# Performance work log

Hardware: AMD Instinct MI355X
Metric: run time of the kernel (lower is better)

Reference implementation:

```python
import jax, jax.numpy as jnp
import numpy as np

K = 3           # kernel_size
PAD = (K - 1) // 2
GC = 16         # group_channels (hardcoded in module)
EPS = 1e-5      # BatchNorm eps


def _extract_patches(x):
    # x: [B,C,H,W] -> [B,C,K*K,H,W], patch index = kh*K+kw (torch Unfold order)
    B, C, H, W = x.shape
    xp = jnp.pad(x, ((0, 0), (0, 0), (PAD, PAD), (PAD, PAD)))
    slices = [xp[:, :, i:i + H, j:j + W] for i in range(K) for j in range(K)]
    return jnp.stack(slices, axis=2)


def setup_inputs() -> dict:
    key = jax.random.key(0)
    ks = jax.random.split(key, 6)
    B, C, H, W = 4, 256, 128, 128
    Cr = C // 4                 # reduction_ratio = 4
    G = C // GC                 # groups = 16
    x = jax.random.normal(ks[0], (B, C, H, W), dtype=jnp.float32)
    # conv1: 1x1, C -> C/4, bias-free (followed by BN) + ReLU
    w1 = jax.random.normal(ks[1], (Cr, C), dtype=jnp.float32) * (1.0 / np.sqrt(C))
    bn_gamma = jnp.ones((Cr,), jnp.float32)
    bn_beta = jnp.zeros((Cr,), jnp.float32)
    bn_mean = jax.random.normal(ks[2], (Cr,), dtype=jnp.float32) * 0.1
    bn_var = jax.random.uniform(ks[3], (Cr,), dtype=jnp.float32, minval=0.5, maxval=1.5)
    # conv2: 1x1, C/4 -> K*K*groups, with bias, no norm/act
    w2 = jax.random.normal(ks[4], (K * K * G, Cr), dtype=jnp.float32) * (1.0 / np.sqrt(Cr))
    b2 = jax.random.normal(ks[5], (K * K * G,), dtype=jnp.float32) * 0.01
    return {"x": x, "w1": w1, "bn_gamma": bn_gamma, "bn_beta": bn_beta,
            "bn_mean": bn_mean, "bn_var": bn_var, "w2": w2, "b2": b2}


def reference(x, w1, bn_gamma, bn_beta, bn_mean, bn_var, w2, b2):
    B, C, H, W = x.shape
    G = C // GC
    # conv1 (1x1) + BN (inference) + ReLU
    h1 = jnp.einsum('bchw,oc->bohw', x, w1)
    inv_std = jax.lax.rsqrt(bn_var + EPS)
    h1 = (h1 - bn_mean[None, :, None, None]) * (bn_gamma * inv_std)[None, :, None, None] \
         + bn_beta[None, :, None, None]
    h1 = jax.nn.relu(h1)
    # conv2 (1x1) -> per-pixel dynamic kernels [B, G, K*K, H, W]
    wk = jnp.einsum('bchw,oc->bohw', h1, w2) + b2[None, :, None, None]
    wk = wk.reshape(B, G, K * K, H, W)
    # unfold x -> [B, G, GC, K*K, H, W], multiply by kernels and reduce over K*K
    patches = _extract_patches(x).reshape(B, G, GC, K * K, H, W)
    out = jnp.einsum('bgkhw,bgckhw->bgchw', wk, patches)
    return out.reshape(B, C, H, W)
```

## Files before the change

kernel.cpp:

```cpp
#include <hip/hip_runtime.h>

#define B_   4
#define C_   256
#define CR_  64
#define H_   128
#define W_   128
#define HW_  (H_ * W_)
#define G_   16
#define GC_  16
#define KO_  144
#define EPS_ 1e-5f

typedef __bf16 bf16x8 __attribute__((ext_vector_type(8)));
typedef __bf16 bf16x4 __attribute__((ext_vector_type(4)));
typedef float  f32x4  __attribute__((ext_vector_type(4)));

#define SX2 132
#define WKS 132

__global__ void prep_kernel(const float* __restrict__ w1,
                            const float* __restrict__ gamma,
                            const float* __restrict__ beta,
                            const float* __restrict__ mean,
                            const float* __restrict__ var,
                            const float* __restrict__ w2,
                            __bf16* __restrict__ w1frag,
                            __bf16* __restrict__ w2frag,
                            float* __restrict__ bias2) {
    int idx = blockIdx.x * 256 + threadIdx.x;
    if (idx < 16384) {
        int kc = idx >> 11, r = idx & 2047;
        int mt = r >> 9, l = (r >> 3) & 63, j = r & 7;
        int o = mt * 16 + (l & 15);
        int c = kc * 32 + 8 * (l >> 4) + j;
        float alpha = gamma[o] * rsqrtf(var[o] + EPS_);
        w1frag[idx] = (__bf16)(w1[o * C_ + c] * alpha);
        if (idx < CR_) {
            float a2 = gamma[idx] * rsqrtf(var[idx] + EPS_);
            bias2[idx] = beta[idx] - mean[idx] * a2;
        }
    } else if (idx < 16384 + 9216) {
        int i2 = idx - 16384;
        int mt = i2 >> 10, r = i2 & 1023;
        int kc2 = r >> 9, l = (r >> 3) & 63, j = r & 7;
        int o2 = mt * 16 + (l & 15);
        int cc = kc2 * 32 + 8 * (l >> 4) + j;
        w2frag[i2] = (__bf16)(w2[o2 * CR_ + cc]);
    }
}

__global__ __launch_bounds__(512, 4) void fused_kernel(
        const float* __restrict__ x,
        const __bf16* __restrict__ w1frag,
        const float* __restrict__ bias2,
        const __bf16* __restrict__ w2frag,
        const float* __restrict__ b2,
        float* __restrict__ out) {
    __shared__ __align__(16) char smem[54912];
    __bf16* wkbuf = (__bf16*)smem;
    __bf16* xs    = (__bf16*)smem;
    __bf16* hbuf  = (__bf16*)(smem + 38016);

    const int tid  = threadIdx.x;
    const int lane = tid & 63;
    const int wave = tid >> 6;
    const int wm = wave >> 2, wn = wave & 3;
    const int g = lane >> 4, n = lane & 15;

    const int bid = (blockIdx.x & 7) * 64 + (blockIdx.x >> 3);
    const int b   = bid >> 7;
    const int h   = bid & 127;

    const float* xrow = x + (size_t)b * C_ * HW_ + h * W_;

#pragma unroll
    for (int i = 0; i < 2; ++i) {
        int s = tid + 512 * i;
        int cl = s >> 5, f4i = s & 31;
        float4 v = *(const float4*)&xrow[(size_t)cl * HW_ + f4i * 4];
        *(bf16x4*)&xs[cl * SX2 + f4i * 4] =
            bf16x4{(__bf16)v.x, (__bf16)v.y, (__bf16)v.z, (__bf16)v.w};
    }
    __syncthreads();

    f32x4 acc1[2][2];
#pragma unroll
    for (int m = 0; m < 2; ++m)
#pragma unroll
        for (int t = 0; t < 2; ++t) acc1[m][t] = f32x4{0.f, 0.f, 0.f, 0.f};

    for (int kc = 0; kc < 8; ++kc) {
        const int buf = kc & 1;
        float4 nf[2];
        if (kc < 7) {
#pragma unroll
            for (int i = 0; i < 2; ++i) {
                int s = tid + 512 * i;
                int cl = s >> 5, f4i = s & 31;
                nf[i] = *(const float4*)&xrow[(size_t)(32 * (kc + 1) + cl) * HW_ + f4i * 4];
            }
        }
        bf16x8 a0 = *(const bf16x8*)&w1frag[((kc * 4 + 2 * wm + 0) * 64 + lane) * 8];
        bf16x8 a1 = *(const bf16x8*)&w1frag[((kc * 4 + 2 * wm + 1) * 64 + lane) * 8];
        const int base = buf * (32 * SX2);
        bf16x8 bt[2];
#pragma unroll
        for (int t = 0; t < 2; ++t)
#pragma unroll
            for (int j = 0; j < 8; ++j)
                bt[t][j] = xs[base + (8 * g + j) * SX2 + (2 * wn + t) * 16 + n];
#pragma unroll
        for (int t = 0; t < 2; ++t) {
            acc1[0][t] = __builtin_amdgcn_mfma_f32_16x16x32_bf16(a0, bt[t], acc1[0][t], 0, 0, 0);
            acc1[1][t] = __builtin_amdgcn_mfma_f32_16x16x32_bf16(a1, bt[t], acc1[1][t], 0, 0, 0);
        }
        if (kc < 7) {
            const int nb = (buf ^ 1) * (32 * SX2);
#pragma unroll
            for (int i = 0; i < 2; ++i) {
                int s = tid + 512 * i;
                int cl = s >> 5, f4i = s & 31;
                *(bf16x4*)&xs[nb + cl * SX2 + f4i * 4] =
                    bf16x4{(__bf16)nf[i].x, (__bf16)nf[i].y, (__bf16)nf[i].z, (__bf16)nf[i].w};
            }
        }
        __syncthreads();
    }

#pragma unroll
    for (int m = 0; m < 2; ++m) {
        const int Mo = (2 * wm + m) * 16 + 4 * g;
        float4 bv = *(const float4*)&bias2[Mo];
        float bj[4] = {bv.x, bv.y, bv.z, bv.w};
#pragma unroll
        for (int t = 0; t < 2; ++t) {
            const int px = (2 * wn + t) * 16 + n;
#pragma unroll
            for (int j = 0; j < 4; ++j)
                hbuf[(Mo + j) * SX2 + px] = (__bf16)fmaxf(acc1[m][t][j] + bj[j], 0.f);
        }
    }
    __syncthreads();

    f32x4 acc2[9];
#pragma unroll
    for (int m = 0; m < 9; ++m) acc2[m] = f32x4{0.f, 0.f, 0.f, 0.f};

#pragma unroll
    for (int kc2 = 0; kc2 < 2; ++kc2) {
        bf16x8 hb;
#pragma unroll
        for (int j = 0; j < 8; ++j)
            hb[j] = hbuf[(kc2 * 32 + 8 * g + j) * SX2 + wave * 16 + n];
#pragma unroll
        for (int mt = 0; mt < 9; ++mt) {
            bf16x8 a = *(const bf16x8*)&w2frag[((mt * 2 + kc2) * 64 + lane) * 8];
            acc2[mt] = __builtin_amdgcn_mfma_f32_16x16x32_bf16(a, hb, acc2[mt], 0, 0, 0);
        }
    }

#pragma unroll
    for (int mt = 0; mt < 9; ++mt) {
        const int o0 = mt * 16 + 4 * g;
        float4 bv = *(const float4*)&b2[o0];
        float bj[4] = {bv.x, bv.y, bv.z, bv.w};
#pragma unroll
        for (int j = 0; j < 4; ++j)
            wkbuf[(o0 + j) * WKS + wave * 16 + n] = (__bf16)(acc2[mt][j] + bj[j]);
    }
    __syncthreads();

    const int q   = lane & 31;
    const int sub = lane >> 5;
    const int w0  = q * 4;
    const bool ql = (q == 0), qr = (q == 31);
    const bool h0ok = (h > 0), h2ok = (h < H_ - 1);

    for (int half = 0; half < 2; ++half) {
        const int gq = 2 * wave + half;
        float4 wk4[9];
#pragma unroll
        for (int k = 0; k < 9; ++k) {
            bf16x4 v = *(const bf16x4*)&wkbuf[(gq * 9 + k) * WKS + w0];
            wk4[k] = float4{(float)v[0], (float)v[1], (float)v[2], (float)v[3]};
        }
        const int cbase = gq * GC_ + sub;

        float4 bufA[3], bufB[3];
        {
            const float* xc = x + ((size_t)(b * C_ + cbase)) * HW_ + (h - 1) * W_ + w0;
            bufA[0] = h0ok ? *(const float4*)xc : float4{0.f, 0.f, 0.f, 0.f};
            bufA[1] = *(const float4*)(xc + W_);
            bufA[2] = h2ok ? *(const float4*)(xc + 2 * W_) : float4{0.f, 0.f, 0.f, 0.f};
        }
#pragma unroll
        for (int p = 0; p < 8; ++p) {
            float4* cur = (p & 1) ? bufB : bufA;
            float4* nxt = (p & 1) ? bufA : bufB;
            if (p < 7) {
                const float* xc = x + ((size_t)(b * C_ + cbase + 2 * (p + 1))) * HW_ + (h - 1) * W_ + w0;
                nxt[0] = h0ok ? *(const float4*)xc : float4{0.f, 0.f, 0.f, 0.f};
                nxt[1] = *(const float4*)(xc + W_);
                nxt[2] = h2ok ? *(const float4*)(xc + 2 * W_) : float4{0.f, 0.f, 0.f, 0.f};
            }
            float4 acc = {0.f, 0.f, 0.f, 0.f};
#pragma unroll
            for (int dr = 0; dr < 3; ++dr) {
                float4 c = cur[dr];
                float lms = __shfl(c.w, lane - 1);
                float rms = __shfl(c.x, lane + 1);
                float lm = ql ? 0.f : lms;
                float rm = qr ? 0.f : rms;
                float4 t0 = wk4[3 * dr + 0];
                float4 t1 = wk4[3 * dr + 1];
                float4 t2 = wk4[3 * dr + 2];
                acc.x = fmaf(t0.x, lm,  acc.x);
                acc.y = fmaf(t0.y, c.x, acc.y);
                acc.z = fmaf(t0.z, c.y, acc.z);
                acc.w = fmaf(t0.w, c.z, acc.w);
                acc.x = fmaf(t1.x, c.x, acc.x);
                acc.y = fmaf(t1.y, c.y, acc.y);
                acc.z = fmaf(t1.z, c.z, acc.z);
                acc.w = fmaf(t1.w, c.w, acc.w);
                acc.x = fmaf(t2.x, c.y, acc.x);
                acc.y = fmaf(t2.y, c.z, acc.y);
                acc.z = fmaf(t2.z, c.w, acc.z);
                acc.w = fmaf(t2.w, rm,  acc.w);
            }
            f32x4 av = {acc.x, acc.y, acc.z, acc.w};
            __builtin_nontemporal_store(av,
                (f32x4*)&out[((size_t)(b * C_ + cbase + 2 * p)) * HW_ + h * W_ + w0]);
        }
    }
}

extern "C" void kernel_launch(void* const* d_in, const int* in_sizes, int n_in,
                              void* d_out, int out_size, void* d_ws, size_t ws_size,
                              hipStream_t stream) {
    const float* x     = (const float*)d_in[0];
    const float* w1    = (const float*)d_in[1];
    const float* gamma = (const float*)d_in[2];
    const float* beta  = (const float*)d_in[3];
    const float* mean  = (const float*)d_in[4];
    const float* var   = (const float*)d_in[5];
    const float* w2    = (const float*)d_in[6];
    const float* b2    = (const float*)d_in[7];
    float* out = (float*)d_out;

    char* ws = (char*)d_ws;
    __bf16* w1frag = (__bf16*)(ws);
    __bf16* w2frag = (__bf16*)(ws + (32 << 10));
    float*  bias2  = (float*)(ws + (56 << 10));

    hipLaunchKernelGGL(prep_kernel, dim3(100), dim3(256), 0, stream,
                       w1, gamma, beta, mean, var, w2, w1frag, w2frag, bias2);
    hipLaunchKernelGGL(fused_kernel, dim3(512), dim3(512), 0, stream,
                       x, w1frag, bias2, w2frag, b2, out);
}
```

Measured before the change: 43.24 us.

## Split each row into quarter-width tiles with smaller blocks and LDS footprint

Each block now handles a 32-pixel quarter of an image row with 256 threads instead of a full 128-pixel row with 512 threads. The grid grows from 512 to 2048 blocks and shared memory shrinks from about 54KB to about 10KB, which is meant to raise occupancy and spread the memory-bound work better across CUs. The conv2 MFMA tiles are split 5/4 across wave pairs, and the depthwise stage fetches halo pixels at tile edges with scalar loads. The cost is redundant halo reads, uneven wave work in conv2, and an extra barrier.

```diff
diff --git a/kernel.cpp b/kernel.cpp
--- a/kernel.cpp
+++ b/kernel.cpp
@@ -15,8 +15,7 @@
 typedef __bf16 bf16x4 __attribute__((ext_vector_type(4)));
 typedef float  f32x4  __attribute__((ext_vector_type(4)));
 
-#define SX2 132
-#define WKS 132
+#define ST 36
 
 __global__ void prep_kernel(const float* __restrict__ w1,
                             const float* __restrict__ gamma,
@@ -49,188 +48,180 @@
     }
 }
 
-__global__ __launch_bounds__(512, 4) void fused_kernel(
+__global__ __launch_bounds__(256, 6) void fused_kernel(
         const float* __restrict__ x,
         const __bf16* __restrict__ w1frag,
         const float* __restrict__ bias2,
         const __bf16* __restrict__ w2frag,
         const float* __restrict__ b2,
         float* __restrict__ out) {
-    __shared__ __align__(16) char smem[54912];
+    __shared__ __align__(16) char smem[10368];
+    __bf16* xs    = (__bf16*)smem;
+    __bf16* hbuf  = (__bf16*)(smem + 4608);
     __bf16* wkbuf = (__bf16*)smem;
-    __bf16* xs    = (__bf16*)smem;
-    __bf16* hbuf  = (__bf16*)(smem + 38016);
 
     const int tid  = threadIdx.x;
     const int lane = tid & 63;
     const int wave = tid >> 6;
-    const int wm = wave >> 2, wn = wave & 3;
     const int g = lane >> 4, n = lane & 15;
 
-    const int bid = (blockIdx.x & 7) * 64 + (blockIdx.x >> 3);
-    const int b   = bid >> 7;
-    const int h   = bid & 127;
-
-    const float* xrow = x + (size_t)b * C_ * HW_ + h * W_;
-
-#pragma unroll
-    for (int i = 0; i < 2; ++i) {
-        int s = tid + 512 * i;
-        int cl = s >> 5, f4i = s & 31;
+    const int bid = (blockIdx.x & 7) * 256 + (blockIdx.x >> 3);
+    const int b   = bid >> 9;
+    const int rem = bid & 511;
+    const int h   = rem >> 2;
+    const int qt  = rem & 3;
+    const int w0g = qt * 32;
+
+    const float* xrow = x + (size_t)b * C_ * HW_ + h * W_ + w0g;
+    const int cl  = tid >> 3;
+    const int f4i = tid & 7;
+
+    {
         float4 v = *(const float4*)&xrow[(size_t)cl * HW_ + f4i * 4];
-        *(bf16x4*)&xs[cl * SX2 + f4i * 4] =
+        *(bf16x4*)&xs[cl * ST + f4i * 4] =
             bf16x4{(__bf16)v.x, (__bf16)v.y, (__bf16)v.z, (__bf16)v.w};
     }
     __syncthreads();
 
-    f32x4 acc1[2][2];
-#pragma unroll
-    for (int m = 0; m < 2; ++m)
-#pragma unroll
-        for (int t = 0; t < 2; ++t) acc1[m][t] = f32x4{0.f, 0.f, 0.f, 0.f};
+    f32x4 acc1[2];
+    acc1[0] = f32x4{0.f, 0.f, 0.f, 0.f};
+    acc1[1] = f32x4{0.f, 0.f, 0.f, 0.f};
 
     for (int kc = 0; kc < 8; ++kc) {
         const int buf = kc & 1;
-        float4 nf[2];
+        float4 nf;
+        if (kc < 7)
+            nf = *(const float4*)&xrow[(size_t)(32 * (kc + 1) + cl) * HW_ + f4i * 4];
+        bf16x8 a = *(const bf16x8*)&w1frag[((kc * 4 + wave) * 64 + lane) * 8];
+        const int base = buf * (32 * ST);
+        bf16x8 bt[2];
+#pragma unroll
+        for (int t = 0; t < 2; ++t)
+#pragma unroll
+            for (int j = 0; j < 8; ++j)
+                bt[t][j] = xs[base + (8 * g + j) * ST + t * 16 + n];
+        acc1[0] = __builtin_amdgcn_mfma_f32_16x16x32_bf16(a, bt[0], acc1[0], 0, 0, 0);
+        acc1[1] = __builtin_amdgcn_mfma_f32_16x16x32_bf16(a, bt[1], acc1[1], 0, 0, 0);
         if (kc < 7) {
-#pragma unroll
-            for (int i = 0; i < 2; ++i) {
-                int s = tid + 512 * i;
-                int cl = s >> 5, f4i = s & 31;
-                nf[i] = *(const float4*)&xrow[(size_t)(32 * (kc + 1) + cl) * HW_ + f4i * 4];
-            }
-        }
-        bf16x8 a0 = *(const bf16x8*)&w1frag[((kc * 4 + 2 * wm + 0) * 64 + lane) * 8];
-        bf16x8 a1 = *(const bf16x8*)&w1frag[((kc * 4 + 2 * wm + 1) * 64 + lane) * 8];
-        const int base = buf * (32 * SX2);
-        bf16x8 bt[2];
-#pragma unroll
-        for (int t = 0; t < 2; ++t)
-#pragma unroll
-            for (int j = 0; j < 8; ++j)
-                bt[t][j] = xs[base + (8 * g + j) * SX2 + (2 * wn + t) * 16 + n];
-#pragma unroll
-        for (int t = 0; t < 2; ++t) {
-            acc1[0][t] = __builtin_amdgcn_mfma_f32_16x16x32_bf16(a0, bt[t], acc1[0][t], 0, 0, 0);
-            acc1[1][t] = __builtin_amdgcn_mfma_f32_16x16x32_bf16(a1, bt[t], acc1[1][t], 0, 0, 0);
-        }
-        if (kc < 7) {
-            const int nb = (buf ^ 1) * (32 * SX2);
-#pragma unroll
-            for (int i = 0; i < 2; ++i) {
-                int s = tid + 512 * i;
-                int cl = s >> 5, f4i = s & 31;
-                *(bf16x4*)&xs[nb + cl * SX2 + f4i * 4] =
-                    bf16x4{(__bf16)nf[i].x, (__bf16)nf[i].y, (__bf16)nf[i].z, (__bf16)nf[i].w};
-            }
+            const int nb = (buf ^ 1) * (32 * ST);
+            *(bf16x4*)&xs[nb + cl * ST + f4i * 4] =
+                bf16x4{(__bf16)nf.x, (__bf16)nf.y, (__bf16)nf.z, (__bf16)nf.w};
         }
         __syncthreads();
     }
 
-#pragma unroll
-    for (int m = 0; m < 2; ++m) {
-        const int Mo = (2 * wm + m) * 16 + 4 * g;
+    {
+        const int Mo = wave * 16 + 4 * g;
         float4 bv = *(const float4*)&bias2[Mo];
         float bj[4] = {bv.x, bv.y, bv.z, bv.w};
 #pragma unroll
-        for (int t = 0; t < 2; ++t) {
-            const int px = (2 * wn + t) * 16 + n;
+        for (int t = 0; t < 2; ++t)
 #pragma unroll
             for (int j = 0; j < 4; ++j)
-                hbuf[(Mo + j) * SX2 + px] = (__bf16)fmaxf(acc1[m][t][j] + bj[j], 0.f);
-        }
-    }
-    __syncthreads();
-
-    f32x4 acc2[9];
-#pragma unroll
-    for (int m = 0; m < 9; ++m) acc2[m] = f32x4{0.f, 0.f, 0.f, 0.f};
+                hbuf[(Mo + j) * ST + t * 16 + n] = (__bf16)fmaxf(acc1[t][j] + bj[j], 0.f);
+    }
+    __syncthreads();
+
+    const int nt = wave & 1;
+    const int mh = wave >> 1;
+    const int nmt = mh ? 4 : 5;
+    const int mt0 = mh ? 5 : 0;
+
+    f32x4 acc2[5];
+#pragma unroll
+    for (int m = 0; m < 5; ++m) acc2[m] = f32x4{0.f, 0.f, 0.f, 0.f};
 
 #pragma unroll
     for (int kc2 = 0; kc2 < 2; ++kc2) {
         bf16x8 hb;
 #pragma unroll
         for (int j = 0; j < 8; ++j)
-            hb[j] = hbuf[(kc2 * 32 + 8 * g + j) * SX2 + wave * 16 + n];
-#pragma unroll
-        for (int mt = 0; mt < 9; ++mt) {
-            bf16x8 a = *(const bf16x8*)&w2frag[((mt * 2 + kc2) * 64 + lane) * 8];
-            acc2[mt] = __builtin_amdgcn_mfma_f32_16x16x32_bf16(a, hb, acc2[mt], 0, 0, 0);
-        }
-    }
-
-#pragma unroll
-    for (int mt = 0; mt < 9; ++mt) {
-        const int o0 = mt * 16 + 4 * g;
+            hb[j] = hbuf[(kc2 * 32 + 8 * g + j) * ST + nt * 16 + n];
+        for (int im = 0; im < nmt; ++im) {
+            bf16x8 a = *(const bf16x8*)&w2frag[(((mt0 + im) * 2 + kc2) * 64 + lane) * 8];
+            acc2[im] = __builtin_amdgcn_mfma_f32_16x16x32_bf16(a, hb, acc2[im], 0, 0, 0);
+        }
+    }
+    __syncthreads();
+
+    for (int im = 0; im < nmt; ++im) {
+        const int o0 = (mt0 + im) * 16 + 4 * g;
         float4 bv = *(const float4*)&b2[o0];
         float bj[4] = {bv.x, bv.y, bv.z, bv.w};
 #pragma unroll
         for (int j = 0; j < 4; ++j)
-            wkbuf[(o0 + j) * WKS + wave * 16 + n] = (__bf16)(acc2[mt][j] + bj[j]);
-    }
-    __syncthreads();
-
-    const int q   = lane & 31;
-    const int sub = lane >> 5;
-    const int w0  = q * 4;
-    const bool ql = (q == 0), qr = (q == 31);
+            wkbuf[(o0 + j) * ST + nt * 16 + n] = (__bf16)(acc2[im][j] + bj[j]);
+    }
+    __syncthreads();
+
+    const int q8 = tid & 7;
+    const int cp = tid >> 3;
+    const int gq = cp >> 1;
+    const int w0 = q8 * 4;
+    const bool lb = (q8 == 0), rb = (q8 == 7);
+    const bool il = (qt == 0), ir = (qt == 3);
     const bool h0ok = (h > 0), h2ok = (h < H_ - 1);
 
-    for (int half = 0; half < 2; ++half) {
-        const int gq = 2 * wave + half;
-        float4 wk4[9];
-#pragma unroll
-        for (int k = 0; k < 9; ++k) {
-            bf16x4 v = *(const bf16x4*)&wkbuf[(gq * 9 + k) * WKS + w0];
-            wk4[k] = float4{(float)v[0], (float)v[1], (float)v[2], (float)v[3]};
-        }
-        const int cbase = gq * GC_ + sub;
-
-        float4 bufA[3], bufB[3];
-        {
-            const float* xc = x + ((size_t)(b * C_ + cbase)) * HW_ + (h - 1) * W_ + w0;
-            bufA[0] = h0ok ? *(const float4*)xc : float4{0.f, 0.f, 0.f, 0.f};
-            bufA[1] = *(const float4*)(xc + W_);
-            bufA[2] = h2ok ? *(const float4*)(xc + 2 * W_) : float4{0.f, 0.f, 0.f, 0.f};
-        }
-#pragma unroll
-        for (int p = 0; p < 8; ++p) {
-            float4* cur = (p & 1) ? bufB : bufA;
-            float4* nxt = (p & 1) ? bufA : bufB;
-            if (p < 7) {
-                const float* xc = x + ((size_t)(b * C_ + cbase + 2 * (p + 1))) * HW_ + (h - 1) * W_ + w0;
-                nxt[0] = h0ok ? *(const float4*)xc : float4{0.f, 0.f, 0.f, 0.f};
-                nxt[1] = *(const float4*)(xc + W_);
-                nxt[2] = h2ok ? *(const float4*)(xc + 2 * W_) : float4{0.f, 0.f, 0.f, 0.f};
-            }
-            float4 acc = {0.f, 0.f, 0.f, 0.f};
-#pragma unroll
-            for (int dr = 0; dr < 3; ++dr) {
-                float4 c = cur[dr];
-                float lms = __shfl(c.w, lane - 1);
-                float rms = __shfl(c.x, lane + 1);
-                float lm = ql ? 0.f : lms;
-                float rm = qr ? 0.f : rms;
-                float4 t0 = wk4[3 * dr + 0];
-                float4 t1 = wk4[3 * dr + 1];
-                float4 t2 = wk4[3 * dr + 2];
-                acc.x = fmaf(t0.x, lm,  acc.x);
-                acc.y = fmaf(t0.y, c.x, acc.y);
-                acc.z = fmaf(t0.z, c.y, acc.z);
-                acc.w = fmaf(t0.w, c.z, acc.w);
-                acc.x = fmaf(t1.x, c.x, acc.x);
-                acc.y = fmaf(t1.y, c.y, acc.y);
-                acc.z = fmaf(t1.z, c.z, acc.z);
-                acc.w = fmaf(t1.w, c.w, acc.w);
-                acc.x = fmaf(t2.x, c.y, acc.x);
-                acc.y = fmaf(t2.y, c.z, acc.y);
-                acc.z = fmaf(t2.z, c.w, acc.z);
-                acc.w = fmaf(t2.w, rm,  acc.w);
-            }
-            f32x4 av = {acc.x, acc.y, acc.z, acc.w};
-            __builtin_nontemporal_store(av,
-                (f32x4*)&out[((size_t)(b * C_ + cbase + 2 * p)) * HW_ + h * W_ + w0]);
-        }
+    float4 wk4[9];
+#pragma unroll
+    for (int k = 0; k < 9; ++k) {
+        bf16x4 v = *(const bf16x4*)&wkbuf[(gq * 9 + k) * ST + w0];
+        wk4[k] = float4{(float)v[0], (float)v[1], (float)v[2], (float)v[3]};
+    }
+
+    const int ch0 = cp * 8;
+    float4 bufA[3], bufB[3];
+    float  eA[3], eB[3];
+
+    auto LOADCH = [&](int ci, float4* bf, float* e) {
+        const float* xc = x + ((size_t)(b * C_ + ch0 + ci)) * HW_ + (h - 1) * W_ + w0g + w0;
+#pragma unroll
+        for (int dr = 0; dr < 3; ++dr) {
+            const bool ok = (dr == 0) ? h0ok : (dr == 2) ? h2ok : true;
+            const float* rp = xc + dr * W_;
+            bf[dr] = ok ? *(const float4*)rp : float4{0.f, 0.f, 0.f, 0.f};
+            e[dr] = 0.f;
+            if (lb && ok && !il) e[dr] = rp[-1];
+            if (rb && ok && !ir) e[dr] = rp[4];
+        }
+    };
+
+    LOADCH(0, bufA, eA);
+#pragma unroll
+    for (int p = 0; p < 8; ++p) {
+        float4* cur = (p & 1) ? bufB : bufA;
+        float*  ecur = (p & 1) ? eB : eA;
+        if (p < 7) {
+            if (p & 1) LOADCH(p + 1, bufA, eA);
+            else       LOADCH(p + 1, bufB, eB);
+        }
+        float4 acc = {0.f, 0.f, 0.f, 0.f};
+#pragma unroll
+        for (int dr = 0; dr < 3; ++dr) {
+            float4 c = cur[dr];
+            float lms = __shfl(c.w, lane - 1);
+            float rms = __shfl(c.x, lane + 1);
+            float lm = lb ? ecur[dr] : lms;
+            float rm = rb ? ecur[dr] : rms;
+            float4 t0 = wk4[3 * dr + 0];
+            float4 t1 = wk4[3 * dr + 1];
+            float4 t2 = wk4[3 * dr + 2];
+            acc.x = fmaf(t0.x, lm,  acc.x);
+            acc.y = fmaf(t0.y, c.x, acc.y);
+            acc.z = fmaf(t0.z, c.y, acc.z);
+            acc.w = fmaf(t0.w, c.z, acc.w);
+            acc.x = fmaf(t1.x, c.x, acc.x);
+            acc.y = fmaf(t1.y, c.y, acc.y);
+            acc.z = fmaf(t1.z, c.z, acc.z);
+            acc.w = fmaf(t1.w, c.w, acc.w);
+            acc.x = fmaf(t2.x, c.y, acc.x);
+            acc.y = fmaf(t2.y, c.z, acc.y);
+            acc.z = fmaf(t2.z, c.w, acc.z);
+            acc.w = fmaf(t2.w, rm,  acc.w);
+        }
+        f32x4 av = {acc.x, acc.y, acc.z, acc.w};
+        __builtin_nontemporal_store(av,
+            (f32x4*)&out[((size_t)(b * C_ + ch0 + p)) * HW_ + h * W_ + w0g + w0]);
     }
 }
 
@@ -254,6 +245,6 @@
 
     hipLaunchKernelGGL(prep_kernel, dim3(100), dim3(256), 0, stream,
                        w1, gamma, beta, mean, var, w2, w1frag, w2frag, bias2);
-    hipLaunchKernelGGL(fused_kernel, dim3(512), dim3(512), 0, stream,
+    hipLaunchKernelGGL(fused_kernel, dim3(2048), dim3(256), 0, stream,
                        x, w1frag, bias2, w2frag, b2, out);
 }
```

Measured after the change: 101.2 us. 2.34x slower.

## Double block size to 1024 threads and redistribute work across 16 waves

Applied to the files above, without the earlier changes.

Launches the fused kernel with 1024 threads per block instead of 512 and splits every phase across 16 waves. Each wave now does half of the conv1 tile, about half of the conv2 M-tiles (5 or 4), and one group of the dynamic-kernel application instead of two. The goal is more parallelism and latency hiding per row block, with fewer registers per thread. The risks are that launch_bounds(1024,8) may be unachievable given the 54.9KB of LDS per block, which can force register spills, and that residency may drop to fewer blocks per CU.

```diff
diff --git a/kernel.cpp b/kernel.cpp
--- a/kernel.cpp
+++ b/kernel.cpp
@@ -49,7 +49,7 @@
     }
 }
 
-__global__ __launch_bounds__(512, 4) void fused_kernel(
+__global__ __launch_bounds__(1024, 8) void fused_kernel(
         const float* __restrict__ x,
         const __bf16* __restrict__ w1frag,
         const float* __restrict__ bias2,
@@ -64,7 +64,6 @@
     const int tid  = threadIdx.x;
     const int lane = tid & 63;
     const int wave = tid >> 6;
-    const int wm = wave >> 2, wn = wave & 3;
     const int g = lane >> 4, n = lane & 15;
 
     const int bid = (blockIdx.x & 7) * 64 + (blockIdx.x >> 3);
@@ -73,100 +72,89 @@
 
     const float* xrow = x + (size_t)b * C_ * HW_ + h * W_;
 
-#pragma unroll
-    for (int i = 0; i < 2; ++i) {
-        int s = tid + 512 * i;
-        int cl = s >> 5, f4i = s & 31;
+    {
+        int cl = tid >> 5, f4i = tid & 31;
         float4 v = *(const float4*)&xrow[(size_t)cl * HW_ + f4i * 4];
         *(bf16x4*)&xs[cl * SX2 + f4i * 4] =
             bf16x4{(__bf16)v.x, (__bf16)v.y, (__bf16)v.z, (__bf16)v.w};
     }
     __syncthreads();
 
-    f32x4 acc1[2][2];
-#pragma unroll
-    for (int m = 0; m < 2; ++m)
-#pragma unroll
-        for (int t = 0; t < 2; ++t) acc1[m][t] = f32x4{0.f, 0.f, 0.f, 0.f};
+    const int wm  = wave >> 2;
+    const int wn2 = wave & 3;
+
+    f32x4 acc1[2];
+    acc1[0] = f32x4{0.f, 0.f, 0.f, 0.f};
+    acc1[1] = f32x4{0.f, 0.f, 0.f, 0.f};
 
     for (int kc = 0; kc < 8; ++kc) {
         const int buf = kc & 1;
-        float4 nf[2];
+        float4 nf;
         if (kc < 7) {
-#pragma unroll
-            for (int i = 0; i < 2; ++i) {
-                int s = tid + 512 * i;
-                int cl = s >> 5, f4i = s & 31;
-                nf[i] = *(const float4*)&xrow[(size_t)(32 * (kc + 1) + cl) * HW_ + f4i * 4];
-            }
-        }
-        bf16x8 a0 = *(const bf16x8*)&w1frag[((kc * 4 + 2 * wm + 0) * 64 + lane) * 8];
-        bf16x8 a1 = *(const bf16x8*)&w1frag[((kc * 4 + 2 * wm + 1) * 64 + lane) * 8];
+            int cl = tid >> 5, f4i = tid & 31;
+            nf = *(const float4*)&xrow[(size_t)(32 * (kc + 1) + cl) * HW_ + f4i * 4];
+        }
+        bf16x8 a = *(const bf16x8*)&w1frag[((kc * 4 + wm) * 64 + lane) * 8];
         const int base = buf * (32 * SX2);
         bf16x8 bt[2];
 #pragma unroll
         for (int t = 0; t < 2; ++t)
 #pragma unroll
             for (int j = 0; j < 8; ++j)
-                bt[t][j] = xs[base + (8 * g + j) * SX2 + (2 * wn + t) * 16 + n];
-#pragma unroll
-        for (int t = 0; t < 2; ++t) {
-            acc1[0][t] = __builtin_amdgcn_mfma_f32_16x16x32_bf16(a0, bt[t], acc1[0][t], 0, 0, 0);
-            acc1[1][t] = __builtin_amdgcn_mfma_f32_16x16x32_bf16(a1, bt[t], acc1[1][t], 0, 0, 0);
-        }
+                bt[t][j] = xs[base + (8 * g + j) * SX2 + (2 * wn2 + t) * 16 + n];
+        acc1[0] = __builtin_amdgcn_mfma_f32_16x16x32_bf16(a, bt[0], acc1[0], 0, 0, 0);
+        acc1[1] = __builtin_amdgcn_mfma_f32_16x16x32_bf16(a, bt[1], acc1[1], 0, 0, 0);
         if (kc < 7) {
             const int nb = (buf ^ 1) * (32 * SX2);
-#pragma unroll
-            for (int i = 0; i < 2; ++i) {
-                int s = tid + 512 * i;
-                int cl = s >> 5, f4i = s & 31;
-                *(bf16x4*)&xs[nb + cl * SX2 + f4i * 4] =
-                    bf16x4{(__bf16)nf[i].x, (__bf16)nf[i].y, (__bf16)nf[i].z, (__bf16)nf[i].w};
-            }
+            int cl = tid >> 5, f4i = tid & 31;
+            *(bf16x4*)&xs[nb + cl * SX2 + f4i * 4] =
+                bf16x4{(__bf16)nf.x, (__bf16)nf.y, (__bf16)nf.z, (__bf16)nf.w};
         }
         __syncthreads();
     }
 
-#pragma unroll
-    for (int m = 0; m < 2; ++m) {
-        const int Mo = (2 * wm + m) * 16 + 4 * g;
+    {
+        const int Mo = wm * 16 + 4 * g;
         float4 bv = *(const float4*)&bias2[Mo];
         float bj[4] = {bv.x, bv.y, bv.z, bv.w};
 #pragma unroll
         for (int t = 0; t < 2; ++t) {
-            const int px = (2 * wn + t) * 16 + n;
+            const int px = (2 * wn2 + t) * 16 + n;
 #pragma unroll
             for (int j = 0; j < 4; ++j)
-                hbuf[(Mo + j) * SX2 + px] = (__bf16)fmaxf(acc1[m][t][j] + bj[j], 0.f);
+                hbuf[(Mo + j) * SX2 + px] = (__bf16)fmaxf(acc1[t][j] + bj[j], 0.f);
         }
     }
     __syncthreads();
 
-    f32x4 acc2[9];
-#pragma unroll
-    for (int m = 0; m < 9; ++m) acc2[m] = f32x4{0.f, 0.f, 0.f, 0.f};
+    const int nt  = wave & 7;
+    const int mh  = wave >> 3;
+    const int nmt = mh ? 4 : 5;
+    const int mt0 = mh ? 5 : 0;
+
+    f32x4 acc2[5];
+#pragma unroll
+    for (int m = 0; m < 5; ++m) acc2[m] = f32x4{0.f, 0.f, 0.f, 0.f};
 
 #pragma unroll
     for (int kc2 = 0; kc2 < 2; ++kc2) {
         bf16x8 hb;
 #pragma unroll
         for (int j = 0; j < 8; ++j)
-            hb[j] = hbuf[(kc2 * 32 + 8 * g + j) * SX2 + wave * 16 + n];
-#pragma unroll
-        for (int mt = 0; mt < 9; ++mt) {
-            bf16x8 a = *(const bf16x8*)&w2frag[((mt * 2 + kc2) * 64 + lane) * 8];
-            acc2[mt] = __builtin_amdgcn_mfma_f32_16x16x32_bf16(a, hb, acc2[mt], 0, 0, 0);
-        }
-    }
-
-#pragma unroll
-    for (int mt = 0; mt < 9; ++mt) {
-        const int o0 = mt * 16 + 4 * g;
+            hb[j] = hbuf[(kc2 * 32 + 8 * g + j) * SX2 + nt * 16 + n];
+        for (int im = 0; im < nmt; ++im) {
+            bf16x8 a = *(const bf16x8*)&w2frag[(((mt0 + im) * 2 + kc2) * 64 + lane) * 8];
+            acc2[im] = __builtin_amdgcn_mfma_f32_16x16x32_bf16(a, hb, acc2[im], 0, 0, 0);
+        }
+    }
+
+    for (int im = 0; im < nmt; ++im) {
+        const int o0 = (mt0 + im) * 16 + 4 * g;
         float4 bv = *(const float4*)&b2[o0];
         float bj[4] = {bv.x, bv.y, bv.z, bv.w};
 #pragma unroll
         for (int j = 0; j < 4; ++j)
-            wkbuf[(o0 + j) * WKS + wave * 16 + n] = (__bf16)(acc2[mt][j] + bj[j]);
+            wkbuf[(o0 + j) * WKS + nt * 16 + n] = (__bf16)(acc2[im][j] + bj[j]);
     }
     __syncthreads();
 
@@ -176,61 +164,59 @@
     const bool ql = (q == 0), qr = (q == 31);
     const bool h0ok = (h > 0), h2ok = (h < H_ - 1);
 
-    for (int half = 0; half < 2; ++half) {
-        const int gq = 2 * wave + half;
-        float4 wk4[9];
-#pragma unroll
-        for (int k = 0; k < 9; ++k) {
-            bf16x4 v = *(const bf16x4*)&wkbuf[(gq * 9 + k) * WKS + w0];
-            wk4[k] = float4{(float)v[0], (float)v[1], (float)v[2], (float)v[3]};
-        }
-        const int cbase = gq * GC_ + sub;
-
-        float4 bufA[3], bufB[3];
-        {
-            const float* xc = x + ((size_t)(b * C_ + cbase)) * HW_ + (h - 1) * W_ + w0;
-            bufA[0] = h0ok ? *(const float4*)xc : float4{0.f, 0.f, 0.f, 0.f};
-            bufA[1] = *(const float4*)(xc + W_);
-            bufA[2] = h2ok ? *(const float4*)(xc + 2 * W_) : float4{0.f, 0.f, 0.f, 0.f};
-        }
-#pragma unroll
-        for (int p = 0; p < 8; ++p) {
-            float4* cur = (p & 1) ? bufB : bufA;
-            float4* nxt = (p & 1) ? bufA : bufB;
-            if (p < 7) {
-                const float* xc = x + ((size_t)(b * C_ + cbase + 2 * (p + 1))) * HW_ + (h - 1) * W_ + w0;
-                nxt[0] = h0ok ? *(const float4*)xc : float4{0.f, 0.f, 0.f, 0.f};
-                nxt[1] = *(const float4*)(xc + W_);
-                nxt[2] = h2ok ? *(const float4*)(xc + 2 * W_) : float4{0.f, 0.f, 0.f, 0.f};
-            }
-            float4 acc = {0.f, 0.f, 0.f, 0.f};
-#pragma unroll
-            for (int dr = 0; dr < 3; ++dr) {
-                float4 c = cur[dr];
-                float lms = __shfl(c.w, lane - 1);
-                float rms = __shfl(c.x, lane + 1);
-                float lm = ql ? 0.f : lms;
-                float rm = qr ? 0.f : rms;
-                float4 t0 = wk4[3 * dr + 0];
-                float4 t1 = wk4[3 * dr + 1];
-                float4 t2 = wk4[3 * dr + 2];
-                acc.x = fmaf(t0.x, lm,  acc.x);
-                acc.y = fmaf(t0.y, c.x, acc.y);
-                acc.z = fmaf(t0.z, c.y, acc.z);
-                acc.w = fmaf(t0.w, c.z, acc.w);
-                acc.x = fmaf(t1.x, c.x, acc.x);
-                acc.y = fmaf(t1.y, c.y, acc.y);
-                acc.z = fmaf(t1.z, c.z, acc.z);
-                acc.w = fmaf(t1.w, c.w, acc.w);
-                acc.x = fmaf(t2.x, c.y, acc.x);
-                acc.y = fmaf(t2.y, c.z, acc.y);
-                acc.z = fmaf(t2.z, c.w, acc.z);
-                acc.w = fmaf(t2.w, rm,  acc.w);
-            }
-            f32x4 av = {acc.x, acc.y, acc.z, acc.w};
-            __builtin_nontemporal_store(av,
-                (f32x4*)&out[((size_t)(b * C_ + cbase + 2 * p)) * HW_ + h * W_ + w0]);
-        }
+    const int gq = wave;
+    float4 wk4[9];
+#pragma unroll
+    for (int k = 0; k < 9; ++k) {
+        bf16x4 v = *(const bf16x4*)&wkbuf[(gq * 9 + k) * WKS + w0];
+        wk4[k] = float4{(float)v[0], (float)v[1], (float)v[2], (float)v[3]};
+    }
+    const int cbase = gq * GC_ + sub;
+
+    float4 bufA[3], bufB[3];
+    {
+        const float* xc = x + ((size_t)(b * C_ + cbase)) * HW_ + (h - 1) * W_ + w0;
+        bufA[0] = h0ok ? *(const float4*)xc : float4{0.f, 0.f, 0.f, 0.f};
+        bufA[1] = *(const float4*)(xc + W_);
+        bufA[2] = h2ok ? *(const float4*)(xc + 2 * W_) : float4{0.f, 0.f, 0.f, 0.f};
+    }
+#pragma unroll
+    for (int p = 0; p < 8; ++p) {
+        float4* cur = (p & 1) ? bufB : bufA;
+        float4* nxt = (p & 1) ? bufA : bufB;
+        if (p < 7) {
+            const float* xc = x + ((size_t)(b * C_ + cbase + 2 * (p + 1))) * HW_ + (h - 1) * W_ + w0;
+            nxt[0] = h0ok ? *(const float4*)xc : float4{0.f, 0.f, 0.f, 0.f};
+            nxt[1] = *(const float4*)(xc + W_);
+            nxt[2] = h2ok ? *(const float4*)(xc + 2 * W_) : float4{0.f, 0.f, 0.f, 0.f};
+        }
+        float4 acc = {0.f, 0.f, 0.f, 0.f};
+#pragma unroll
+        for (int dr = 0; dr < 3; ++dr) {
+            float4 c = cur[dr];
+            float lms = __shfl(c.w, lane - 1);
+            float rms = __shfl(c.x, lane + 1);
+            float lm = ql ? 0.f : lms;
+            float rm = qr ? 0.f : rms;
+            float4 t0 = wk4[3 * dr + 0];
+            float4 t1 = wk4[3 * dr + 1];
+            float4 t2 = wk4[3 * dr + 2];
+            acc.x = fmaf(t0.x, lm,  acc.x);
+            acc.y = fmaf(t0.y, c.x, acc.y);
+            acc.z = fmaf(t0.z, c.y, acc.z);
+            acc.w = fmaf(t0.w, c.z, acc.w);
+            acc.x = fmaf(t1.x, c.x, acc.x);
+            acc.y = fmaf(t1.y, c.y, acc.y);
+            acc.z = fmaf(t1.z, c.z, acc.z);
+            acc.w = fmaf(t1.w, c.w, acc.w);
+            acc.x = fmaf(t2.x, c.y, acc.x);
+            acc.y = fmaf(t2.y, c.z, acc.y);
+            acc.z = fmaf(t2.z, c.w, acc.z);
+            acc.w = fmaf(t2.w, rm,  acc.w);
+        }
+        f32x4 av = {acc.x, acc.y, acc.z, acc.w};
+        __builtin_nontemporal_store(av,
+            (f32x4*)&out[((size_t)(b * C_ + cbase + 2 * p)) * HW_ + h * W_ + w0]);
     }
 }
 
@@ -254,6 +240,6 @@
 
     hipLaunchKernelGGL(prep_kernel, dim3(100), dim3(256), 0, stream,
                        w1, gamma, beta, mean, var, w2, w1frag, w2frag, bias2);
-    hipLaunchKernelGGL(fused_kernel, dim3(512), dim3(512), 0, stream,
+    hipLaunchKernelGGL(fused_kernel, dim3(512), dim3(1024), 0, stream,
                        x, w1frag, bias2, w2frag, b2, out);
 }
```

Measured after the change: 143.7 us. +232.2%, slower.
